# Kernel tuning notes

Measured on AMD Instinct MI355X. Metric: run time of the kernel, lower is better.

## Reference

```python
import jax, jax.numpy as jnp
import numpy as np

B, N, P, D, K = 32, 512, 25, 128, 64
PROMPT_THRESHOLD = 0.5
T_MTI = 24  # last time patch is masked (module asserts t_mti == [24])


def setup_inputs() -> dict:
    key = jax.random.key(0)
    k1, k2, k3, k4, k5 = jax.random.split(key, 5)
    patches = jax.random.normal(k1, (B, N, P, D), dtype=jnp.float32)
    # kaiming-uniform-like init scale for the embedding tables
    scale = 1.0 / np.sqrt(D)
    u_prompt = jax.random.normal(k2, (K, D), dtype=jnp.float32) * scale
    m_prompt = jax.random.normal(k3, (K, D), dtype=jnp.float32) * scale
    s_mti = jnp.sort(jax.random.randint(k4, (256,), 0, N))
    s_uti = jnp.sort(jax.random.randint(k5, (256,), 0, N))
    return {"patches": patches, "u_prompt": u_prompt, "m_prompt": m_prompt,
            "s_mti": s_mti, "s_uti": s_uti}


def reference(patches, u_prompt, m_prompt, s_mti, s_uti):
    n, p = patches.shape[1], patches.shape[2]
    # multiplicative masks equivalent to score_map[:, s_mti] = 0 and score_map[:, :, 24] = 0
    n_mask = jnp.ones((n,), dtype=patches.dtype).at[s_mti].set(0.0)
    t_mask = jnp.ones((p,), dtype=patches.dtype).at[T_MTI].set(0.0)
    keep = (n_mask[:, None] * t_mask[None, :])[None, :, :, None]  # [1,N,P,1]

    # --- unmasked-prompt pass ---
    su = jax.nn.sigmoid(jnp.einsum('bnpd,kd->bnpk', patches, u_prompt))
    su = su * (su > PROMPT_THRESHOLD).astype(su.dtype) * keep
    out = patches + jnp.einsum('bnpk,kd->bnpd', su, u_prompt)

    # --- masked-prompt pass: score - score_with_keep == score * (1 - keep) ---
    sm = jax.nn.sigmoid(jnp.einsum('bnpd,kd->bnpk', patches, m_prompt))
    sm = sm * (sm > PROMPT_THRESHOLD).astype(sm.dtype) * (1.0 - keep)
    out = out + jnp.einsum('bnpk,kd->bnpd', sm, m_prompt)
    return out
```

## Files before the change

### kernel.cpp

```cpp
#include <hip/hip_runtime.h>


constexpr int NN = 512;
constexpr int PP = 25;
constexpr int DD = 128;
constexpr int KK = 64;
constexpr int THREADS = 512;
constexpr int ROWS = 32 * NN * PP;
constexpr int RPB = THREADS / 4;
constexpr int BLOCKS = ROWS / RPB;

__global__ __launch_bounds__(THREADS, 4)
void ape_kernel(const float* __restrict__ patches,
                const float* __restrict__ u_prompt,
                const float* __restrict__ m_prompt,
                const int* __restrict__ s_mti,
                float* __restrict__ out)
{
    __shared__ float Eu[KK * DD];
    __shared__ float Em[KK * DD];
    __shared__ unsigned nmask[NN / 32];

    const int tid = threadIdx.x;

    if (tid < NN / 32) nmask[tid] = 0u;
    __syncthreads();
    if (tid < 256) {
        int idx = s_mti[tid];
        atomicOr(&nmask[idx >> 5], 1u << (idx & 31));
    }
    {
        const float4* u4 = reinterpret_cast<const float4*>(u_prompt);
        const float4* m4 = reinterpret_cast<const float4*>(m_prompt);
        float4* a4 = reinterpret_cast<float4*>(Eu);
        float4* b4 = reinterpret_cast<float4*>(Em);
#pragma unroll
        for (int i = 0; i < (KK * DD / 4) / THREADS; ++i) {
            a4[i * THREADS + tid] = u4[i * THREADS + tid];
            b4[i * THREADS + tid] = m4[i * THREADS + tid];
        }
    }
    __syncthreads();

    const int q = tid & 3;
    const int r = blockIdx.x * RPB + (tid >> 2);
    const int rdp = r / PP;
    const int pp = r - rdp * PP;
    const int n = rdp & (NN - 1);
    const bool masked = (((nmask[n >> 5] >> (n & 31)) & 1u) != 0u) || (pp == 24);
    const float* Eb = (masked ? Em : Eu) + q * 32;

    const float4* pr = reinterpret_cast<const float4*>(patches) + (size_t)r * 32 + q * 8;
    float4 row[8], acc[8];
#pragma unroll
    for (int t = 0; t < 8; ++t) {
        int o = (t + 2 * q) & 7;
        row[t] = pr[o];
        acc[t] = row[t];
    }

#pragma unroll 1
    for (int k = 0; k < KK; ++k) {
        const float4* ek = reinterpret_cast<const float4*>(Eb + k * DD);
        float4 e[8];
        float a0 = 0.f, a1 = 0.f, a2 = 0.f, a3 = 0.f;
#pragma unroll
        for (int t = 0; t < 8; ++t) {
            int o = (t + 2 * q) & 7;
            e[t] = ek[o];
            a0 = fmaf(row[t].x, e[t].x, a0);
            a1 = fmaf(row[t].y, e[t].y, a1);
            a2 = fmaf(row[t].z, e[t].z, a2);
            a3 = fmaf(row[t].w, e[t].w, a3);
        }
        float lg = (a0 + a1) + (a2 + a3);
        lg += __shfl_xor(lg, 1);
        lg += __shfl_xor(lg, 2);

        float g;
        if (__any(__builtin_fabsf(lg) < 1e-3f)) {
            double dd = 0.0;
#pragma unroll
            for (int t = 0; t < 8; ++t) {
                dd = fma((double)row[t].x, (double)e[t].x, dd);
                dd = fma((double)row[t].y, (double)e[t].y, dd);
                dd = fma((double)row[t].z, (double)e[t].z, dd);
                dd = fma((double)row[t].w, (double)e[t].w, dd);
            }
            dd += __shfl_xor(dd, 1);
            dd += __shfl_xor(dd, 2);
            if (fabs(dd) < 4e-5) {
                g = 0.25f;
            } else if (dd > 0.0) {
                g = 1.0f / (1.0f + __expf(-lg));
            } else {
                g = 0.0f;
            }
        } else {
            g = (lg > 0.0f) ? (1.0f / (1.0f + __expf(-lg))) : 0.0f;
        }

#pragma unroll
        for (int t = 0; t < 8; ++t) {
            acc[t].x = fmaf(g, e[t].x, acc[t].x);
            acc[t].y = fmaf(g, e[t].y, acc[t].y);
            acc[t].z = fmaf(g, e[t].z, acc[t].z);
            acc[t].w = fmaf(g, e[t].w, acc[t].w);
        }
    }

    float4* po = reinterpret_cast<float4*>(out) + (size_t)r * 32 + q * 8;
#pragma unroll
    for (int t = 0; t < 8; ++t) {
        int o = (t + 2 * q) & 7;
        po[o] = acc[t];
    }
}

extern "C" void kernel_launch(void* const* d_in, const int* in_sizes, int n_in,
                              void* d_out, int out_size, void* d_ws, size_t ws_size,
                              hipStream_t stream) {
    const float* patches  = (const float*)d_in[0];
    const float* u_prompt = (const float*)d_in[1];
    const float* m_prompt = (const float*)d_in[2];
    const int*   s_mti    = (const int*)d_in[3];
    float* outp = (float*)d_out;

    ape_kernel<<<BLOCKS, THREADS, 0, stream>>>(patches, u_prompt, m_prompt, s_mti, outp);
}
```

Before: 671.7 us.

## Swizzle LDS prompt tables and stage output through shared memory for coalesced stores

Merges the two prompt tables into one swizzled LDS buffer so the per-k reads from the four lanes of a row avoid bank conflicts, and loads each patch row in linear order. After the loop the accumulators are written to the now-free LDS with an XOR swizzle and read back so each global store is fully coalesced across the block. The sigmoid division becomes a hardware reciprocal, and the launch-bounds occupancy hint drops from 4 to 2 blocks per CU. This trades two extra barriers and an LDS round trip for better global write coalescing, and the lower occupancy hint may change register allocation.

```diff
diff --git a/kernel.cpp b/kernel.cpp
--- a/kernel.cpp
+++ b/kernel.cpp
@@ -10,18 +10,18 @@
 constexpr int RPB = THREADS / 4;
 constexpr int BLOCKS = ROWS / RPB;
 
-__global__ __launch_bounds__(THREADS, 4)
+__global__ __launch_bounds__(THREADS, 2)
 void ape_kernel(const float* __restrict__ patches,
                 const float* __restrict__ u_prompt,
                 const float* __restrict__ m_prompt,
                 const int* __restrict__ s_mti,
                 float* __restrict__ out)
 {
-    __shared__ float Eu[KK * DD];
-    __shared__ float Em[KK * DD];
+    __shared__ float S[2 * KK * DD];
     __shared__ unsigned nmask[NN / 32];
 
     const int tid = threadIdx.x;
+    float4* S4 = reinterpret_cast<float4*>(S);
 
     if (tid < NN / 32) nmask[tid] = 0u;
     __syncthreads();
@@ -29,45 +29,50 @@
         int idx = s_mti[tid];
         atomicOr(&nmask[idx >> 5], 1u << (idx & 31));
     }
+
     {
         const float4* u4 = reinterpret_cast<const float4*>(u_prompt);
         const float4* m4 = reinterpret_cast<const float4*>(m_prompt);
-        float4* a4 = reinterpret_cast<float4*>(Eu);
-        float4* b4 = reinterpret_cast<float4*>(Em);
 #pragma unroll
-        for (int i = 0; i < (KK * DD / 4) / THREADS; ++i) {
-            a4[i * THREADS + tid] = u4[i * THREADS + tid];
-            b4[i * THREADS + tid] = m4[i * THREADS + tid];
+        for (int i = 0; i < 4; ++i) {
+            int jj = i * THREADS + tid;
+            int k = jj >> 5, j = jj & 31;
+            int phys = (j & 24) | ((j ^ (j >> 3)) & 7);
+            S4[k * 32 + phys]        = u4[jj];
+            S4[2048 + k * 32 + phys] = m4[jj];
         }
     }
     __syncthreads();
 
     const int q = tid & 3;
-    const int r = blockIdx.x * RPB + (tid >> 2);
+    const int rl = tid >> 2;
+    const int r = blockIdx.x * RPB + rl;
     const int rdp = r / PP;
     const int pp = r - rdp * PP;
     const int n = rdp & (NN - 1);
     const bool masked = (((nmask[n >> 5] >> (n & 31)) & 1u) != 0u) || (pp == 24);
-    const float* Eb = (masked ? Em : Eu) + q * 32;
+    const int tb = masked ? 2048 : 0;
+
+    int ecol[8];
+#pragma unroll
+    for (int t = 0; t < 8; ++t) ecol[t] = tb + q * 8 + ((t ^ q) & 7);
 
     const float4* pr = reinterpret_cast<const float4*>(patches) + (size_t)r * 32 + q * 8;
     float4 row[8], acc[8];
 #pragma unroll
     for (int t = 0; t < 8; ++t) {
-        int o = (t + 2 * q) & 7;
-        row[t] = pr[o];
+        row[t] = pr[t];
         acc[t] = row[t];
     }
 
 #pragma unroll 1
     for (int k = 0; k < KK; ++k) {
-        const float4* ek = reinterpret_cast<const float4*>(Eb + k * DD);
+        const int kb = k * 32;
         float4 e[8];
         float a0 = 0.f, a1 = 0.f, a2 = 0.f, a3 = 0.f;
 #pragma unroll
         for (int t = 0; t < 8; ++t) {
-            int o = (t + 2 * q) & 7;
-            e[t] = ek[o];
+            e[t] = S4[kb + ecol[t]];
             a0 = fmaf(row[t].x, e[t].x, a0);
             a1 = fmaf(row[t].y, e[t].y, a1);
             a2 = fmaf(row[t].z, e[t].z, a2);
@@ -92,12 +97,12 @@
             if (fabs(dd) < 4e-5) {
                 g = 0.25f;
             } else if (dd > 0.0) {
-                g = 1.0f / (1.0f + __expf(-lg));
+                g = __builtin_amdgcn_rcpf(1.0f + __expf(-lg));
             } else {
                 g = 0.0f;
             }
         } else {
-            g = (lg > 0.0f) ? (1.0f / (1.0f + __expf(-lg))) : 0.0f;
+            g = (lg > 0.0f) ? __builtin_amdgcn_rcpf(1.0f + __expf(-lg)) : 0.0f;
         }
 
 #pragma unroll
@@ -109,11 +114,24 @@
         }
     }
 
-    float4* po = reinterpret_cast<float4*>(out) + (size_t)r * 32 + q * 8;
+    __syncthreads();
+    {
+        const int r7 = rl & 7;
+        const int wb = rl * 32 + q * 8;
 #pragma unroll
-    for (int t = 0; t < 8; ++t) {
-        int o = (t + 2 * q) & 7;
-        po[o] = acc[t];
+        for (int t = 0; t < 8; ++t)
+            S4[wb + ((t ^ q ^ r7) & 7)] = acc[t];
+    }
+    __syncthreads();
+    {
+        float4* out4 = reinterpret_cast<float4*>(out) + (size_t)blockIdx.x * (RPB * 32);
+#pragma unroll
+        for (int i = 0; i < 8; ++i) {
+            int flat = i * THREADS + tid;
+            int rr = flat >> 5, c = flat & 31;
+            int qq = c >> 3, tt = c & 7;
+            out4[flat] = S4[rr * 32 + qq * 8 + ((tt ^ qq ^ (rr & 7)) & 7)];
+        }
     }
 }
 
```

After: 659.7 us. No clear change (-1.8%).
